# Optimization experiments

Measured on AMD Instinct MI355X. Metric: run time of the kernel, lower is better.

## Reference

```python
import jax, jax.numpy as jnp
import numpy as np

NUM_SAMPLES = 2048
MAX_AGENTS = 64
D_MODEL = 128
NUM_HEADS = 8


def setup_inputs() -> dict:
    key = jax.random.key(0)
    # deterministic ragged sizes: 1..64 repeating -> total = 32 * (64*65/2) = 66560
    agents = ((np.arange(NUM_SAMPLES) % MAX_AGENTS) + 1).astype(np.int32)
    total = int(agents.sum())
    k1, k2, k3 = jax.random.split(key, 3)
    s = 1.0 / np.sqrt(D_MODEL)
    return {
        "att_in": jax.random.normal(k1, (total, D_MODEL), jnp.float32),
        "in_proj_w": jax.random.uniform(k2, (3 * D_MODEL, D_MODEL), jnp.float32, -s, s),
        "in_proj_b": jnp.zeros((3 * D_MODEL,), jnp.float32),
        "out_proj_w": jax.random.uniform(k3, (D_MODEL, D_MODEL), jnp.float32, -s, s),
        "out_proj_b": jnp.zeros((D_MODEL,), jnp.float32),
        "agents_per_sample": jnp.asarray(agents),
    }


def reference(att_in, in_proj_w, in_proj_b, out_proj_w, out_proj_b, agents_per_sample):
    # agents_per_sample is static ragged metadata (host ints)
    agents = np.asarray(agents_per_sample)
    B = len(agents)
    A = int(agents.max())
    D = att_in.shape[-1]
    hd = D // NUM_HEADS

    # scatter ragged tokens into zero-padded [B, A, D]
    sample_ids = np.repeat(np.arange(B), agents)
    pos = np.concatenate([np.arange(n) for n in agents])
    padded = jnp.zeros((B, A, D), att_in.dtype).at[sample_ids, pos].set(att_in)
    key_valid = jnp.asarray(np.arange(A)[None, :] < agents[:, None])  # [B, A]

    # torch nn.MultiheadAttention math (eval mode, dropout=0)
    qkv = padded @ in_proj_w.T + in_proj_b  # [B, A, 3D]
    q, k, v = jnp.split(qkv, 3, axis=-1)
    q = q.reshape(B, A, NUM_HEADS, hd)
    k = k.reshape(B, A, NUM_HEADS, hd)
    v = v.reshape(B, A, NUM_HEADS, hd)

    scores = jnp.einsum("bqhd,bkhd->bhqk", q, k) / jnp.sqrt(jnp.asarray(hd, q.dtype))
    scores = jnp.where(key_valid[:, None, None, :], scores, jnp.asarray(-1e30, scores.dtype))
    attn = jax.nn.softmax(scores, axis=-1)

    out = jnp.einsum("bhqk,bkhd->bqhd", attn, v).reshape(B, A, D)
    out = out @ out_proj_w.T + out_proj_b

    # unpad: concatenation of the per-sample ragged outputs
    return out[sample_ids, pos]
```

## Files before the change

kernel.cpp:

```cpp
#include <hip/hip_runtime.h>

#define DM 128

typedef __attribute__((ext_vector_type(8))) __bf16 bf16x8;
typedef __attribute__((ext_vector_type(4))) float f32x4;

__device__ inline unsigned short f2bf(float f) {
    unsigned u = __float_as_uint(f);
    u += 0x7FFFu + ((u >> 16) & 1u);
    return (unsigned short)(u >> 16);
}

__global__ void prep(const int* __restrict__ agents, int B, int M,
                     const float* __restrict__ wqkv, const float* __restrict__ wout,
                     const float* __restrict__ x,
                     int* __restrict__ offs,
                     unsigned short* __restrict__ wqkv_bf,
                     unsigned short* __restrict__ wout_bf,
                     unsigned short* __restrict__ xbf) {
    if (blockIdx.x < 64) {
        int idx = (blockIdx.x * 256 + threadIdx.x) * 4;
        if (idx < 49152) {
            float4 v = *(const float4*)(wqkv + idx);
            ushort4 o;
            o.x = f2bf(v.x); o.y = f2bf(v.y); o.z = f2bf(v.z); o.w = f2bf(v.w);
            *(ushort4*)(wqkv_bf + idx) = o;
        } else {
            int j = idx - 49152;
            float4 v = *(const float4*)(wout + j);
            ushort4 o;
            o.x = f2bf(v.x); o.y = f2bf(v.y); o.z = f2bf(v.z); o.w = f2bf(v.w);
            *(ushort4*)(wout_bf + j) = o;
        }
    } else if (blockIdx.x == 64) {
        __shared__ int part[256];
        const int tid = threadIdx.x;
        const int per = (B + 255) >> 8;
        const int base = tid * per;
        int s = 0;
        for (int i = 0; i < per; ++i) {
            int idx = base + i;
            if (idx < B) s += agents[idx];
        }
        part[tid] = s;
        __syncthreads();
        for (int off = 1; off < 256; off <<= 1) {
            int v = (tid >= off) ? part[tid - off] : 0;
            __syncthreads();
            part[tid] += v;
            __syncthreads();
        }
        int run = (tid == 0) ? 0 : part[tid - 1];
        for (int i = 0; i < per; ++i) {
            int idx = base + i;
            if (idx < B) { offs[idx] = run; run += agents[idx]; }
        }
    } else {
        const int nf4 = M * 32;
        const int stride = ((int)gridDim.x - 65) * 256;
        for (int idx = ((int)blockIdx.x - 65) * 256 + (int)threadIdx.x; idx < nf4;
             idx += stride) {
            float4 v = ((const float4*)x)[idx];
            ushort4 o;
            o.x = f2bf(v.x); o.y = f2bf(v.y); o.z = f2bf(v.z); o.w = f2bf(v.w);
            ((ushort4*)xbf)[idx] = o;
        }
    }
}

template<int NT>
__device__ __forceinline__ void qa_body(
    const unsigned short* __restrict__ xbf,
    const unsigned short* __restrict__ wqkvb,
    const float* __restrict__ bqkv,
    unsigned short* __restrict__ obuf,
    int n, int base, int M, int h, int quad, int l16)
{
    constexpr int G   = (NT + 1) / 2;
    constexpr int KT2 = 2 * G;
    bf16x8 qf[NT], kf[NT], vA[G];
    #pragma unroll
    for (int g = 0; g < G; ++g) vA[g] = (bf16x8)(__bf16)0.0f;

    bf16x8 wfq[4], wfk[4], wfv[4];
    const unsigned short* wq = wqkvb + (size_t)(h * 16 + l16) * 128;
    #pragma unroll
    for (int ks = 0; ks < 4; ++ks) {
        wfq[ks] = *(const bf16x8*)(wq + ks * 32 + quad * 8);
        wfk[ks] = *(const bf16x8*)(wq + 128 * 128 + ks * 32 + quad * 8);
        wfv[ks] = *(const bf16x8*)(wq + 256 * 128 + ks * 32 + quad * 8);
    }
    const float4 bq4 = *(const float4*)(bqkv + h * 16 + quad * 4);
    const float4 bk4 = *(const float4*)(bqkv + 128 + h * 16 + quad * 4);
    const float  bv  = bqkv[256 + h * 16 + l16];

    const int shA = (quad & 1) * 32 + l16;
    const int shB = shA + 16;

    #pragma unroll
    for (int mt = 0; mt < NT; ++mt) {
        int row = base + mt * 16 + l16;
        row = row < M ? row : M - 1;
        const unsigned short* xr = xbf + (size_t)row * 128;
        bf16x8 xf[4];
        #pragma unroll
        for (int ks = 0; ks < 4; ++ks)
            xf[ks] = *(const bf16x8*)(xr + ks * 32 + quad * 8);
        f32x4 qa = {0.f,0.f,0.f,0.f}, ka = {0.f,0.f,0.f,0.f}, va = {0.f,0.f,0.f,0.f};
        #pragma unroll
        for (int ks = 0; ks < 4; ++ks) {
            qa = __builtin_amdgcn_mfma_f32_16x16x32_bf16(wfq[ks], xf[ks], qa, 0, 0, 0);
            ka = __builtin_amdgcn_mfma_f32_16x16x32_bf16(wfk[ks], xf[ks], ka, 0, 0, 0);
            va = __builtin_amdgcn_mfma_f32_16x16x32_bf16(xf[ks], wfv[ks], va, 0, 0, 0);
        }
        {
            ushort4 w;
            w.x = f2bf(qa[0] + bq4.x); w.y = f2bf(qa[1] + bq4.y);
            w.z = f2bf(qa[2] + bq4.z); w.w = f2bf(qa[3] + bq4.w);
            unsigned u0 = (unsigned)w.x | ((unsigned)w.y << 16);
            unsigned u1 = (unsigned)w.z | ((unsigned)w.w << 16);
            uint4 q;
            q.x = __shfl(u0, shA); q.y = __shfl(u1, shA);
            q.z = __shfl(u0, shB); q.w = __shfl(u1, shB);
            qf[mt] = (quad < 2) ? __builtin_bit_cast(bf16x8, q) : (bf16x8)(__bf16)0.0f;
        }
        {
            ushort4 w;
            w.x = f2bf(ka[0] + bk4.x); w.y = f2bf(ka[1] + bk4.y);
            w.z = f2bf(ka[2] + bk4.z); w.w = f2bf(ka[3] + bk4.w);
            unsigned u0 = (unsigned)w.x | ((unsigned)w.y << 16);
            unsigned u1 = (unsigned)w.z | ((unsigned)w.w << 16);
            uint4 q;
            q.x = __shfl(u0, shA); q.y = __shfl(u1, shA);
            q.z = __shfl(u0, shB); q.w = __shfl(u1, shB);
            kf[mt] = (quad < 2) ? __builtin_bit_cast(bf16x8, q) : (bf16x8)(__bf16)0.0f;
        }
        #pragma unroll
        for (int r = 0; r < 4; ++r)
            vA[mt >> 1][(mt & 1) * 4 + r] = (__bf16)(va[r] + bv);
    }

    int thr[KT2];
    #pragma unroll
    for (int kt = 0; kt < KT2; ++kt) {
        int t = n - kt * 16 - quad * 4;
        thr[kt] = t < 0 ? 0 : (t > 4 ? 4 : t);
    }
    const float SC2 = 0.25f * 1.44269504088896340736f;

    #pragma unroll
    for (int mt = 0; mt < NT; ++mt) {
        float pr[KT2][4];
        float mm = -3.0e38f;
        #pragma unroll
        for (int kt = 0; kt < KT2; ++kt) {
            if (kt < NT) {
                f32x4 sc = __builtin_amdgcn_mfma_f32_16x16x32_bf16(
                    kf[kt], qf[mt], (f32x4){0.f, 0.f, 0.f, 0.f}, 0, 0, 0);
                #pragma unroll
                for (int r = 0; r < 4; ++r) {
                    float v = sc[r] * SC2;
                    pr[kt][r] = v;
                    mm = fmaxf(mm, v);
                }
            } else {
                #pragma unroll
                for (int r = 0; r < 4; ++r) pr[kt][r] = -3.0e38f;
            }
        }
        mm = fmaxf(mm, __shfl_xor(mm, 16));
        mm = fmaxf(mm, __shfl_xor(mm, 32));
        float ll = 0.f;
        #pragma unroll
        for (int kt = 0; kt < KT2; ++kt)
            #pragma unroll
            for (int r = 0; r < 4; ++r) {
                float e = exp2f(pr[kt][r] - mm);
                e = (r < thr[kt]) ? e : 0.f;
                pr[kt][r] = e;
                ll += e;
            }
        ll += __shfl_xor(ll, 16);
        ll += __shfl_xor(ll, 32);
        float inv = __builtin_amdgcn_rcpf(ll);
        bf16x8 pf[G];
        #pragma unroll
        for (int g = 0; g < G; ++g)
            #pragma unroll
            for (int j = 0; j < 8; ++j)
                pf[g][j] = (__bf16)(pr[2 * g + (j >> 2)][j & 3] * inv);
        f32x4 o = __builtin_amdgcn_mfma_f32_16x16x32_bf16(
            vA[0], pf[0], (f32x4){0.f, 0.f, 0.f, 0.f}, 0, 0, 0);
        if constexpr (G == 2)
            o = __builtin_amdgcn_mfma_f32_16x16x32_bf16(vA[1], pf[1], o, 0, 0, 0);
        const int row = mt * 16 + l16;
        if (row < n) {
            ushort4 w;
            w.x = f2bf(o[0]); w.y = f2bf(o[1]); w.z = f2bf(o[2]); w.w = f2bf(o[3]);
            *(ushort4*)(obuf + (size_t)(base + row) * 256 + h * 16 + quad * 4) = w;
        }
    }
}

__launch_bounds__(64, 3)
__global__ void qkvattn(const unsigned short* __restrict__ xbf,
                        const unsigned short* __restrict__ wqkvb,
                        const float* __restrict__ bqkv,
                        unsigned short* __restrict__ obuf,
                        const int* __restrict__ agents,
                        const int* __restrict__ offs,
                        int M, int B) {
    const int bid = blockIdx.x;
    const int h = bid / B;
    const int s = bid - h * B;
    const int n = agents[s];
    const int base = offs[s];
    const int lane = threadIdx.x & 63, quad = lane >> 4, l16 = lane & 15;
    const int nt = (n + 15) >> 4;
    if      (nt == 1) qa_body<1>(xbf, wqkvb, bqkv, obuf, n, base, M, h, quad, l16);
    else if (nt == 2) qa_body<2>(xbf, wqkvb, bqkv, obuf, n, base, M, h, quad, l16);
    else if (nt == 3) qa_body<3>(xbf, wqkvb, bqkv, obuf, n, base, M, h, quad, l16);
    else              qa_body<4>(xbf, wqkvb, bqkv, obuf, n, base, M, h, quad, l16);
}

__launch_bounds__(256, 4)
__global__ void oproj(const unsigned short* __restrict__ attn_b,
                      const unsigned short* __restrict__ woutb,
                      const float* __restrict__ bout,
                      float* __restrict__ out, int M) {
    __shared__ __align__(16) unsigned short Ws[128 * 136];
    __shared__ __align__(16) float biass[128];
    const int m0 = blockIdx.x * 64;
    const int tid = threadIdx.x;

    for (int f = tid; f < 2048; f += 256) {
        int t = f >> 4, c = f & 15;
        *(uint4*)&Ws[t * 136 + c * 8] = *(const uint4*)(woutb + (size_t)t * 128 + c * 8);
    }
    if (tid < 32)
        ((float4*)biass)[tid] = ((const float4*)bout)[tid];
    __syncthreads();

    const int wave = tid >> 6, lane = tid & 63, quad = lane >> 4, l16 = lane & 15;
    const int mw = m0 + wave * 16;

    bf16x8 af[4];
    {
        int row = mw + l16;
        row = (row < M) ? row : (M - 1);
        #pragma unroll
        for (int ks = 0; ks < 4; ++ks)
            af[ks] = *(const bf16x8*)(attn_b + (size_t)row * 256 + ks * 32 + quad * 8);
    }

    const int row0 = mw + l16;

    for (int ct = 0; ct < 8; ++ct) {
        bf16x8 bc[4];
        #pragma unroll
        for (int ks = 0; ks < 4; ++ks)
            bc[ks] = *(const bf16x8*)&Ws[(ct * 16 + l16) * 136 + ks * 32 + quad * 8];
        f32x4 a0 = {0.f, 0.f, 0.f, 0.f};
        #pragma unroll
        for (int ks = 0; ks < 4; ++ks)
            a0 = __builtin_amdgcn_mfma_f32_16x16x32_bf16(bc[ks], af[ks], a0, 0, 0, 0);
        const int n0 = ct * 16 + quad * 4;
        const float4 b4 = *(const float4*)(biass + n0);
        float4 o0;
        o0.x = a0[0] + b4.x; o0.y = a0[1] + b4.y; o0.z = a0[2] + b4.z; o0.w = a0[3] + b4.w;
        if (row0 < M) *(float4*)(out + (size_t)row0 * DM + n0) = o0;
    }
}

extern "C" void kernel_launch(void* const* d_in, const int* in_sizes, int n_in,
                              void* d_out, int out_size, void* d_ws, size_t ws_size,
                              hipStream_t stream) {
    const float* att_in     = (const float*)d_in[0];
    const float* in_proj_w  = (const float*)d_in[1];
    const float* in_proj_b  = (const float*)d_in[2];
    const float* out_proj_w = (const float*)d_in[3];
    const float* out_proj_b = (const float*)d_in[4];
    const int*   agents     = (const int*)d_in[5];
    const int B = in_sizes[5];
    const int M = out_size / DM;

    int* offs = (int*)d_ws;
    unsigned short* wqkv_bf = (unsigned short*)((char*)d_ws + 8192);
    unsigned short* wout_bf = (unsigned short*)((char*)d_ws + 106496);
    unsigned short* xbf     = (unsigned short*)((char*)d_ws + 139264);
    unsigned short* obuf    = (unsigned short*)d_out;

    hipLaunchKernelGGL(prep, dim3(65 + 1024), dim3(256), 0, stream,
                       agents, B, M, in_proj_w, out_proj_w, att_in,
                       offs, wqkv_bf, wout_bf, xbf);
    hipLaunchKernelGGL(qkvattn, dim3(B * 8), dim3(64), 0, stream,
                       xbf, wqkv_bf, in_proj_b, obuf, agents, offs, M, B);
    hipLaunchKernelGGL(oproj, dim3((M + 63) / 64), dim3(256), 0, stream,
                       obuf, wout_bf, out_proj_b, (float*)d_out, M);
}
```

Baseline: 159.6 us.

## Batch eight samples per attention wave with double-buffered x prefetch

Result: no change. 158.3 us (-0.8%).

```diff
diff --git a/kernel.cpp b/kernel.cpp
--- a/kernel.cpp
+++ b/kernel.cpp
@@ -68,44 +68,56 @@
     }
 }
 
-template<int NT>
-__device__ __forceinline__ void qa_body(
+template<int NTC>
+__device__ __forceinline__ void load_pre(
+    bf16x8 (&xp)[2][4], const unsigned short* __restrict__ xbf,
+    int base, int M, int quad, int l16)
+{
+    constexpr int PRE = NTC < 2 ? NTC : 2;
+    #pragma unroll
+    for (int mt = 0; mt < PRE; ++mt) {
+        int row = base + mt * 16 + l16;
+        row = row < M ? row : M - 1;
+        const unsigned short* xr = xbf + (size_t)row * 128;
+        #pragma unroll
+        for (int ks = 0; ks < 4; ++ks)
+            xp[mt][ks] = *(const bf16x8*)(xr + ks * 32 + quad * 8);
+    }
+}
+
+template<int NTC>
+__device__ __forceinline__ void process_sample(
+    const bf16x8 (&xp)[2][4],
     const unsigned short* __restrict__ xbf,
-    const unsigned short* __restrict__ wqkvb,
-    const float* __restrict__ bqkv,
+    const bf16x8 (&wfq)[4], const bf16x8 (&wfk)[4], const bf16x8 (&wfv)[4],
+    const float4 bq4, const float4 bk4, const float bv,
     unsigned short* __restrict__ obuf,
     int n, int base, int M, int h, int quad, int l16)
 {
-    constexpr int G   = (NT + 1) / 2;
+    constexpr int PRE = NTC < 2 ? NTC : 2;
+    constexpr int G   = (NTC + 1) / 2;
     constexpr int KT2 = 2 * G;
-    bf16x8 qf[NT], kf[NT], vA[G];
-    #pragma unroll
-    for (int g = 0; g < G; ++g) vA[g] = (bf16x8)(__bf16)0.0f;
-
-    bf16x8 wfq[4], wfk[4], wfv[4];
-    const unsigned short* wq = wqkvb + (size_t)(h * 16 + l16) * 128;
-    #pragma unroll
-    for (int ks = 0; ks < 4; ++ks) {
-        wfq[ks] = *(const bf16x8*)(wq + ks * 32 + quad * 8);
-        wfk[ks] = *(const bf16x8*)(wq + 128 * 128 + ks * 32 + quad * 8);
-        wfv[ks] = *(const bf16x8*)(wq + 256 * 128 + ks * 32 + quad * 8);
-    }
-    const float4 bq4 = *(const float4*)(bqkv + h * 16 + quad * 4);
-    const float4 bk4 = *(const float4*)(bqkv + 128 + h * 16 + quad * 4);
-    const float  bv  = bqkv[256 + h * 16 + l16];
-
-    const int shA = (quad & 1) * 32 + l16;
-    const int shB = shA + 16;
-
-    #pragma unroll
-    for (int mt = 0; mt < NT; ++mt) {
+    constexpr int NL  = (NTC > PRE) ? (NTC - PRE) : 1;
+
+    bf16x8 xl[NL][4];
+    #pragma unroll
+    for (int mt = PRE; mt < NTC; ++mt) {
         int row = base + mt * 16 + l16;
         row = row < M ? row : M - 1;
         const unsigned short* xr = xbf + (size_t)row * 128;
-        bf16x8 xf[4];
-        #pragma unroll
-        for (int ks = 0; ks < 4; ++ks)
-            xf[ks] = *(const bf16x8*)(xr + ks * 32 + quad * 8);
+        #pragma unroll
+        for (int ks = 0; ks < 4; ++ks)
+            xl[mt - PRE][ks] = *(const bf16x8*)(xr + ks * 32 + quad * 8);
+    }
+
+    bf16x8 qf[NTC], kf[NTC], vA[G];
+    #pragma unroll
+    for (int g = 0; g < G; ++g) vA[g] = (bf16x8)(__bf16)0.0f;
+    const int shA = (quad & 1) * 32 + l16, shB = shA + 16;
+
+    #pragma unroll
+    for (int mt = 0; mt < NTC; ++mt) {
+        const bf16x8* xf = (mt < PRE) ? xp[mt] : xl[(mt >= PRE) ? (mt - PRE) : 0];
         f32x4 qa = {0.f,0.f,0.f,0.f}, ka = {0.f,0.f,0.f,0.f}, va = {0.f,0.f,0.f,0.f};
         #pragma unroll
         for (int ks = 0; ks < 4; ++ks) {
@@ -149,14 +161,14 @@
     const float SC2 = 0.25f * 1.44269504088896340736f;
 
     #pragma unroll
-    for (int mt = 0; mt < NT; ++mt) {
+    for (int mt = 0; mt < NTC; ++mt) {
         float pr[KT2][4];
         float mm = -3.0e38f;
         #pragma unroll
         for (int kt = 0; kt < KT2; ++kt) {
-            if (kt < NT) {
+            if (kt < NTC) {
                 f32x4 sc = __builtin_amdgcn_mfma_f32_16x16x32_bf16(
-                    kf[kt], qf[mt], (f32x4){0.f, 0.f, 0.f, 0.f}, 0, 0, 0);
+                    kf[(kt < NTC) ? kt : 0], qf[mt], (f32x4){0.f, 0.f, 0.f, 0.f}, 0, 0, 0);
                 #pragma unroll
                 for (int r = 0; r < 4; ++r) {
                     float v = sc[r] * SC2;
@@ -202,25 +214,78 @@
     }
 }
 
-__launch_bounds__(64, 3)
+template<int NTC>
+__device__ __forceinline__ void chunk_body(
+    const unsigned short* __restrict__ xbf,
+    const unsigned short* __restrict__ wqkvb,
+    const float* __restrict__ bqkv,
+    unsigned short* __restrict__ obuf,
+    const int* __restrict__ agents, const int* __restrict__ offs,
+    int s0, int Bn, int M, int h, int quad, int l16)
+{
+    bf16x8 wfq[4], wfk[4], wfv[4];
+    const unsigned short* wq = wqkvb + (size_t)(h * 16 + l16) * 128;
+    #pragma unroll
+    for (int ks = 0; ks < 4; ++ks) {
+        wfq[ks] = *(const bf16x8*)(wq + ks * 32 + quad * 8);
+        wfk[ks] = *(const bf16x8*)(wq + 128 * 128 + ks * 32 + quad * 8);
+        wfv[ks] = *(const bf16x8*)(wq + 256 * 128 + ks * 32 + quad * 8);
+    }
+    const float4 bq4 = *(const float4*)(bqkv + h * 16 + quad * 4);
+    const float4 bk4 = *(const float4*)(bqkv + 128 + h * 16 + quad * 4);
+    const float  bv  = bqkv[256 + h * 16 + l16];
+
+    int ns[8], bs[8];
+    #pragma unroll
+    for (int i = 0; i < 8; ++i) {
+        int s = s0 + i;
+        ns[i] = (s < Bn) ? agents[s] : 0;
+        bs[i] = (s < Bn) ? offs[s] : 0;
+    }
+
+    bf16x8 xA[2][4], xB[2][4];
+    load_pre<NTC>(xA, xbf, bs[0], M, quad, l16);
+    #pragma unroll
+    for (int i = 0; i < 8; i += 2) {
+        if (i + 1 < 8) load_pre<NTC>(xB, xbf, bs[i + 1], M, quad, l16);
+        if (ns[i] > 0)
+            process_sample<NTC>(xA, xbf, wfq, wfk, wfv, bq4, bk4, bv,
+                                obuf, ns[i], bs[i], M, h, quad, l16);
+        if (i + 2 < 8) load_pre<NTC>(xA, xbf, bs[i + 2], M, quad, l16);
+        if (ns[i + 1] > 0)
+            process_sample<NTC>(xB, xbf, wfq, wfk, wfv, bq4, bk4, bv,
+                                obuf, ns[i + 1], bs[i + 1], M, h, quad, l16);
+    }
+}
+
+__launch_bounds__(64, 2)
 __global__ void qkvattn(const unsigned short* __restrict__ xbf,
                         const unsigned short* __restrict__ wqkvb,
                         const float* __restrict__ bqkv,
                         unsigned short* __restrict__ obuf,
                         const int* __restrict__ agents,
                         const int* __restrict__ offs,
-                        int M, int B) {
+                        int M, int Bn) {
     const int bid = blockIdx.x;
-    const int h = bid / B;
-    const int s = bid - h * B;
-    const int n = agents[s];
-    const int base = offs[s];
+    const int h = bid & 7;
+    const int fld = bid >> 3;
+    const int nch = (Bn + 7) >> 3;
+    const int c = (nch == 256) ? (((fld & 31) << 3) | (fld >> 5)) : fld;
+    const int s0 = c * 8;
     const int lane = threadIdx.x & 63, quad = lane >> 4, l16 = lane & 15;
-    const int nt = (n + 15) >> 4;
-    if      (nt == 1) qa_body<1>(xbf, wqkvb, bqkv, obuf, n, base, M, h, quad, l16);
-    else if (nt == 2) qa_body<2>(xbf, wqkvb, bqkv, obuf, n, base, M, h, quad, l16);
-    else if (nt == 3) qa_body<3>(xbf, wqkvb, bqkv, obuf, n, base, M, h, quad, l16);
-    else              qa_body<4>(xbf, wqkvb, bqkv, obuf, n, base, M, h, quad, l16);
+
+    int nmax = 0;
+    #pragma unroll
+    for (int i = 0; i < 8; ++i) {
+        int s = s0 + i;
+        int v = (s < Bn) ? agents[s] : 0;
+        nmax = v > nmax ? v : nmax;
+    }
+    const int ntc = (nmax + 15) >> 4;
+    if      (ntc <= 1) chunk_body<1>(xbf, wqkvb, bqkv, obuf, agents, offs, s0, Bn, M, h, quad, l16);
+    else if (ntc == 2) chunk_body<2>(xbf, wqkvb, bqkv, obuf, agents, offs, s0, Bn, M, h, quad, l16);
+    else if (ntc == 3) chunk_body<3>(xbf, wqkvb, bqkv, obuf, agents, offs, s0, Bn, M, h, quad, l16);
+    else               chunk_body<4>(xbf, wqkvb, bqkv, obuf, agents, offs, s0, Bn, M, h, quad, l16);
 }
 
 __launch_bounds__(256, 4)
@@ -290,10 +355,12 @@
     unsigned short* xbf     = (unsigned short*)((char*)d_ws + 139264);
     unsigned short* obuf    = (unsigned short*)d_out;
 
+    const int nch = (B + 7) >> 3;
+
     hipLaunchKernelGGL(prep, dim3(65 + 1024), dim3(256), 0, stream,
                        agents, B, M, in_proj_w, out_proj_w, att_in,
                        offs, wqkv_bf, wout_bf, xbf);
-    hipLaunchKernelGGL(qkvattn, dim3(B * 8), dim3(64), 0, stream,
+    hipLaunchKernelGGL(qkvattn, dim3(nch * 8), dim3(64), 0, stream,
                        xbf, wqkv_bf, in_proj_b, obuf, agents, offs, M, B);
     hipLaunchKernelGGL(oproj, dim3((M + 63) / 64), dim3(256), 0, stream,
                        obuf, wout_bf, out_proj_b, (float*)d_out, M);
```
